# Performance work log

Measured on AMD Instinct MI355X. Metric: run time of the kernel, lower is better.

## Reference

```python
import jax, jax.numpy as jnp
import numpy as np

# Config matching init_kwargs: 63 single-grapheme tokens + optional blank -> C = 64,
# trivial (identity) lexicon, ngram = 0 (no transition model), allow_repeats = True.
# Under this config the GTN composition (target chain o lexicon -> tokens graph ->
# alignments, intersected with linear emission graph, forward_score) is exactly the
# CTC forward algorithm over the extended label sequence z = [blank, y1, blank, ...,
# yL, blank], with the s-2 -> s skip allowed for ALL non-blank states (allow_repeats).

B, T, C, L = 128, 3000, 64, 128
NEG = -1e30  # effective -inf, safe in fp32


def setup_inputs() -> dict:
    key = jax.random.key(0)
    k1, k2 = jax.random.split(key)
    inputs = jax.random.normal(k1, (B, T, C), dtype=jnp.float32)  # raw logits
    # target token ids in [0, C-2]; blank = C-1 is never a target
    targets = jax.random.randint(k2, (B, L), 0, C - 1, dtype=jnp.int32)
    return {"inputs": inputs, "targets": targets}


def reference(inputs, targets):
    Bv, Tv, Cv = inputs.shape
    Lv = targets.shape[1]
    S = 2 * Lv + 1
    blank = Cv - 1
    # transitions is None -> module applies log_softmax to inputs
    logp = jax.nn.log_softmax(inputs, axis=2)  # [B, T, C]
    # extended label sequence: blanks at even positions, targets at odd positions
    z = jnp.full((Bv, S), blank, dtype=jnp.int32).at[:, 1::2].set(targets)  # [B, S]
    # per-frame emission scores for each extended state: [B, T, S] -> [T, B, S]
    em = jnp.take_along_axis(logp, jnp.broadcast_to(z[:, None, :], (Bv, Tv, S)), axis=2)
    em = jnp.transpose(em, (1, 0, 2))
    # skip transition (s-2 -> s) allowed for every non-blank (odd) state because
    # allow_repeats=True (no z[s] != z[s-2] restriction)
    skip_ok = (jnp.arange(S) % 2 == 1)  # [S]

    alpha0 = (jnp.full((Bv, S), NEG, dtype=jnp.float32)
              .at[:, 0].set(em[0, :, 0])
              .at[:, 1].set(em[0, :, 1]))

    def step(alpha, e_t):
        a1 = jnp.pad(alpha[:, :-1], ((0, 0), (1, 0)), constant_values=NEG)
        a2 = jnp.pad(alpha[:, :-2], ((0, 0), (2, 0)), constant_values=NEG)
        a2 = jnp.where(skip_ok[None, :], a2, NEG)
        new = e_t + jax.scipy.special.logsumexp(jnp.stack([alpha, a1, a2], axis=0), axis=0)
        return new, None

    alphaT, _ = jax.lax.scan(step, alpha0, em[1:])  # [B, S]
    # accepting states: last label (S-2) and trailing blank (S-1)
    ll = jax.scipy.special.logsumexp(alphaT[:, S - 2:S], axis=1)  # [B]
    # reduction='none' -> scales = 1; forward returns torch.mean over batch
    return jnp.mean(-ll)
```

## Files before the change

kernel.cpp:

```cpp
#include <hip/hip_runtime.h>
#include <stdint.h>

#define BB 128
#define TT 3000
#define CC 64
#define LL 128
#define NEGf (-1e30f)
#define LOG2E 1.4426950408889634f
#define LN2f 0.6931471805599453f
#define F 12
#define NCH 250
#define NPH (NCH + 1)
#define NULLM (-30000)
#define LSE_BLOCKS 512

typedef float f32x2 __attribute__((ext_vector_type(2)));
typedef float f32x4 __attribute__((ext_vector_type(4)));

__device__ __forceinline__ float fexp2(float x){ return __builtin_amdgcn_exp2f(x); }
__device__ __forceinline__ float flog2(float x){ return __builtin_amdgcn_logf(x); }
__device__ __forceinline__ int dpp_shr1_i(int x, int old){
    return __builtin_amdgcn_update_dpp(old, x, 0x138, 0xF, 0xF, false);
}
__device__ __forceinline__ float dpp_shr1_f(float x, float old){
    int r = __builtin_amdgcn_update_dpp(__float_as_int(old), __float_as_int(x),
                                        0x138, 0xF, 0xF, false);
    return __int_as_float(r);
}
#define DPPMAXT(x,c) fmaxf((x),__int_as_float(__builtin_amdgcn_update_dpp(0,__float_as_int(x),(c),0xF,0xF,true)))
#define DPPADDT(x,c) ((x)+__int_as_float(__builtin_amdgcn_update_dpp(0,__float_as_int(x),(c),0xF,0xF,true)))
#define RED64(OP,x) { x=OP(x,0x111); x=OP(x,0x112); x=OP(x,0x114); x=OP(x,0x118); x=OP(x,0x142); x=OP(x,0x143); }

__global__ __launch_bounds__(512) void fused_kernel(const float* __restrict__ in,
                                                    const int* __restrict__ tgt,
                                                    float* __restrict__ lse,
                                                    float* __restrict__ ll2){
    __shared__ __align__(16) float emR[3][F][258];
    __shared__ __align__(16) float bndR[3][F][2];
    __shared__ __align__(16) float nullBnd[24];
    __shared__ float laL[3008];
    __shared__ float lbL[3008];
    if (blockIdx.x < BB) {
        const int b = blockIdx.x;
        const int wave = threadIdx.x >> 6;
        const int lane = threadIdx.x & 63;
        const float* fb = in + (size_t)b * TT * CC;
        const uint32_t em_base  = (uint32_t)(uintptr_t)&emR[0][0][0];
        const uint32_t bnd_base = (uint32_t)(uintptr_t)&bndR[0][0][0];

        if (wave < 2) {
            const int W = wave;
            __builtin_amdgcn_s_setprio(1);
            if (W == 0) {
                if (lane < 12) { nullBnd[2*lane] = __int_as_float(NULLM); nullBnd[2*lane+1] = 0.5f; }
                if (lane == 0) { bndR[0][0][0] = __int_as_float(NULLM); bndR[0][0][1] = 0.5f; }
                if (lane < 8) { laL[3000+lane] = NEGf; lbL[3000+lane] = 0.f; }
            }
            int a0m = NULLM, a1m = NULLM; float a0r = 0.5f, a1r = 0.5f;
            if (W == 0 && lane == 0) { a0m = 1; a0r = 0.5f; }
            const uint32_t em1_ad = em_base + (uint32_t)((64*W + lane) * 8);
            const uint32_t emB_ad = em_base + 1024u;
            const uint32_t nb_ad  = (uint32_t)(uintptr_t)&nullBnd[0];
            __syncthreads();
            for (int ph = 0; ph < NPH; ++ph) {
                const int x = ph - W;
                if (x >= 0 && x < NCH) {
                    const uint32_t buf = (uint32_t)(x % 3);
                    const uint32_t ra = em1_ad + buf*12384u;
                    const uint32_t rb = emB_ad + buf*12384u;
                    const uint32_t rq = W ? (bnd_base + buf*96u) : nb_ad;
                    f32x4 B4[6]; f32x2 E1[F], EB[F];
                    asm volatile("ds_read_b128 %0, %1 offset:0"  : "=v"(B4[0]) : "v"(rq));
                    asm volatile("ds_read_b128 %0, %1 offset:16" : "=v"(B4[1]) : "v"(rq));
                    asm volatile("ds_read_b128 %0, %1 offset:32" : "=v"(B4[2]) : "v"(rq));
                    asm volatile("ds_read_b128 %0, %1 offset:48" : "=v"(B4[3]) : "v"(rq));
                    asm volatile("ds_read_b128 %0, %1 offset:64" : "=v"(B4[4]) : "v"(rq));
                    asm volatile("ds_read_b128 %0, %1 offset:80" : "=v"(B4[5]) : "v"(rq));
                    asm volatile("ds_read_b64 %0, %1 offset:0"    : "=v"(E1[0]) : "v"(ra));
                    asm volatile("ds_read_b64 %0, %1 offset:0"    : "=v"(EB[0]) : "v"(rb));
                    asm volatile("ds_read_b64 %0, %1 offset:1032" : "=v"(E1[1]) : "v"(ra));
                    asm volatile("ds_read_b64 %0, %1 offset:1032" : "=v"(EB[1]) : "v"(rb));
                    asm volatile("ds_read_b64 %0, %1 offset:2064" : "=v"(E1[2]) : "v"(ra));
                    asm volatile("ds_read_b64 %0, %1 offset:2064" : "=v"(EB[2]) : "v"(rb));
                    int hm[F]; float hr[F];
                    #pragma unroll
                    for (int j = 0; j < F; ++j) {
                        if (j + 3 < F) {
                            asm volatile("ds_read_b64 %0, %1 offset:%2"
                                         : "=v"(E1[j+3]) : "v"(ra), "n"((j+3)*1032));
                            asm volatile("ds_read_b64 %0, %1 offset:%2"
                                         : "=v"(EB[j+3]) : "v"(rb), "n"((j+3)*1032));
                            asm volatile("s_waitcnt lgkmcnt(6)" ::: "memory");
                        } else if (j + 3 == F) {
                            asm volatile("s_waitcnt lgkmcnt(4)" ::: "memory");
                        } else if (j + 2 == F) {
                            asm volatile("s_waitcnt lgkmcnt(2)" ::: "memory");
                        } else {
                            asm volatile("s_waitcnt lgkmcnt(0)" ::: "memory");
                        }
                        __builtin_amdgcn_sched_barrier(0);
                        const int   bjm = __float_as_int((j&1) ? B4[j>>1].z : B4[j>>1].x);
                        const float bjr = (j&1) ? B4[j>>1].w : B4[j>>1].y;
                        const int   e1m = __float_as_int(E1[j].x); const float e1r = E1[j].y;
                        const int   ebm = __float_as_int(EB[j].x); const float ebr = EB[j].y;
                        int p1m = dpp_shr1_i(a1m, NULLM);
                        float p1r = dpp_shr1_f(a1r, 0.5f);
                        p1m = (lane == 0) ? bjm : p1m;
                        p1r = (lane == 0) ? bjr : p1r;
                        int Mt = (a0m > p1m) ? a0m : p1m;
                        float rs = ldexpf(a0r, a0m - Mt) + ldexpf(p1r, p1m - Mt);
                        int ui = __float_as_int(rs);
                        int n0m = Mt + ((ui >> 23) - 126) + ebm;
                        float n0r = __int_as_float((ui & 0x7FFFFF) | 0x3F000000) * ebr;
                        int Mu = (a1m > a0m) ? a1m : a0m; Mu = (Mu > p1m) ? Mu : p1m;
                        float ru = ldexpf(a1r, a1m - Mu) + ldexpf(a0r, a0m - Mu)
                                 + ldexpf(p1r, p1m - Mu);
                        int uj = __float_as_int(ru);
                        int n1m = Mu + ((uj >> 23) - 126) + e1m;
                        float n1r = __int_as_float((uj & 0x7FFFFF) | 0x3F000000) * e1r;
                        a0m = n0m; a0r = n0r; a1m = n1m; a1r = n1r;
                        hm[j] = a1m; hr[j] = a1r;
                    }
                    if (W == 0 && lane == 63) {
                        float* s0 = &bndR[x % 3][0][0];
                        #pragma unroll
                        for (int j = 0; j < F-1; ++j) {
                            s0[(j+1)*2] = __int_as_float(hm[j]); s0[(j+1)*2+1] = hr[j];
                        }
                        float* s1 = &bndR[(x+1) % 3][0][0];
                        s1[0] = __int_as_float(hm[F-1]); s1[1] = hr[F-1];
                    }
                    if (W == 1 && lane == 63) {
                        #pragma unroll
                        for (int j = 0; j < F; ++j)
                            laL[x*F + j] = (float)hm[j] + flog2(hr[j]);
                    }
                    asm volatile("s_waitcnt lgkmcnt(0)" ::: "memory");
                }
                __syncthreads();
            }
            __syncthreads();
            if (W == 0) {
                const int base = lane*47;
                float seg = 0.f;
                for (int k = 0; k < 47; ++k) seg += lbL[base+k];
                float inc = seg;
                #pragma unroll
                for (int d = 1; d < 64; d <<= 1) {
                    float t = __shfl_up(inc, d, 64);
                    if (lane >= d) inc += t;
                }
                float CBtot = __int_as_float(__builtin_amdgcn_readlane(__float_as_int(inc), 63));
                float ex = inc - seg;
                float cb = ex, gm = NEGf;
                for (int k = 0; k < 47; ++k) {
                    int idx = base+k;
                    cb += lbL[idx];
                    float g = laL[idx] + (CBtot - cb);
                    g = (idx == 2999) ? NEGf : g;
                    gm = fmaxf(gm, g);
                }
                RED64(DPPMAXT, gm);
                float gmax = __int_as_float(__builtin_amdgcn_readlane(__float_as_int(gm), 63));
                cb = ex; float se = 0.f;
                for (int k = 0; k < 47; ++k) {
                    int idx = base+k;
                    cb += lbL[idx];
                    float g = laL[idx] + (CBtot - cb);
                    g = (idx == 2999) ? NEGf : g;
                    se += fexp2(g - gmax);
                }
                RED64(DPPADDT, se);
                float S = __int_as_float(__builtin_amdgcn_readlane(__float_as_int(se), 63));
                float la256 = gmax + flog2(S);
                float la255f = laL[2999];
                float m = fmaxf(la255f, la256);
                float r = m + flog2(1.0f + fexp2(-fabsf(la255f - la256)));
                if (lane == 0) ll2[b] = r;
            }
        } else {
            const int p = wave - 2;
            const int t0 = tgt[b*LL + lane];
            const int t1 = tgt[b*LL + 64 + lane];
            float v0[2], v1[2], vb[2];
            auto loadc = [&](int cc){
                const float* cbase = fb + (size_t)cc * F * CC;
                #pragma unroll
                for (int k = 0; k < 2; ++k) {
                    const float* fr = cbase + (p + 6*k) * CC;
                    v0[k] = fr[t0]; v1[k] = fr[t1]; vb[k] = fr[63];
                }
            };
            auto storec = [&](int cc){
                const int buf = cc % 3;
                #pragma unroll
                for (int k = 0; k < 2; ++k) {
                    const int f = p + 6*k;
                    float x0 = v0[k] * LOG2E; float f0 = floorf(x0);
                    *(f32x2*)&emR[buf][f][2*lane] =
                        (f32x2){__int_as_float((int)f0 + 1), fexp2(x0 - f0 - 1.0f)};
                    float x1 = v1[k] * LOG2E; float f1 = floorf(x1);
                    *(f32x2*)&emR[buf][f][2*(64+lane)] =
                        (f32x2){__int_as_float((int)f1 + 1), fexp2(x1 - f1 - 1.0f)};
                    if (lane == 0) {
                        float xb = vb[k] * LOG2E; float fbl = floorf(xb);
                        *(f32x2*)&emR[buf][f][256] =
                            (f32x2){__int_as_float((int)fbl + 1), fexp2(xb - fbl - 1.0f)};
                        lbL[cc*F + f] = xb;
                    }
                }
            };
            loadc(0); storec(0); loadc(1);
            __syncthreads();
            for (int ph = 0; ph < NPH; ++ph) {
                if (ph + 1 < NCH) storec(ph + 1);
                if (ph + 2 < NCH) loadc(ph + 2);
                __syncthreads();
            }
            __syncthreads();
        }
        return;
    }
    int wv = (blockIdx.x - BB) * 8 + (threadIdx.x >> 6);
    int lane = threadIdx.x & 63;
    const int stride = LSE_BLOCKS * 8;
    for (int row = wv; row < BB * TT; row += stride) {
        float x = in[(size_t)row * CC + lane];
        float m = x;
        #pragma unroll
        for (int d = 32; d >= 1; d >>= 1) m = fmaxf(m, __shfl_xor(m, d, 64));
        float s = fexp2((x - m) * LOG2E);
        #pragma unroll
        for (int d = 32; d >= 1; d >>= 1) s += __shfl_xor(s, d, 64);
        if (lane == 0) lse[row] = m + flog2(s) * LN2f;
    }
}

__global__ __launch_bounds__(256) void bsum_kernel(const float* __restrict__ lse,
                                                   const float* __restrict__ ll2,
                                                   float* __restrict__ lossb) {
    __shared__ float red[256];
    int b = blockIdx.x;
    float s = 0.f;
    for (int i = threadIdx.x; i < TT; i += 256) s += lse[(size_t)b * TT + i];
    red[threadIdx.x] = s;
    __syncthreads();
    #pragma unroll
    for (int w = 128; w >= 1; w >>= 1) {
        if (threadIdx.x < w) red[threadIdx.x] += red[threadIdx.x + w];
        __syncthreads();
    }
    if (threadIdx.x == 0) lossb[b] = red[0] - ll2[b] * LN2f;
}

__global__ __launch_bounds__(64) void final_kernel(const float* __restrict__ lossb,
                                                   float* __restrict__ out) {
    int lane = threadIdx.x;
    float v = lossb[lane] + lossb[lane + 64];
    #pragma unroll
    for (int d = 32; d >= 1; d >>= 1) v += __shfl_xor(v, d, 64);
    if (lane == 0) out[0] = v / (float)BB;
}

extern "C" void kernel_launch(void* const* d_in, const int* in_sizes, int n_in,
                              void* d_out, int out_size, void* d_ws, size_t ws_size,
                              hipStream_t stream) {
    const float* in = (const float*)d_in[0];
    const int* tg = (const int*)d_in[1];
    float* out = (float*)d_out;
    float* lse = (float*)d_ws;
    float* ll2 = lse + (size_t)BB * TT;
    float* lossb = ll2 + BB;

    hipLaunchKernelGGL(fused_kernel, dim3(BB + LSE_BLOCKS), dim3(512), 0, stream,
                       in, tg, lse, ll2);
    hipLaunchKernelGGL(bsum_kernel, dim3(BB), dim3(256), 0, stream, lse, ll2, lossb);
    hipLaunchKernelGGL(final_kernel, dim3(1), dim3(64), 0, stream, lossb, out);
}
```

Before: 280.7 us.

## Replace per-chunk block barriers with LDS flag-based producer/consumer pipeline

Removes the __syncthreads per chunk between the two alpha-recursion waves and the six emission-loading waves. Coordination now uses LDS counters and flags with spin-wait polling, a 4-slot emission ring and a 5-slot boundary ring, so the two recursion waves can run a chunk apart without a full-block barrier. Emissions are stored as plain fp32 exp2 scales (one float per state instead of an exponent/mantissa pair), and each step folds the emission in with a multiply before renormalising. The log conversion of the saved alphas moves into the final reduction. The cost is extra polling traffic and s_sleep latency, plus a risk of subtle ordering bugs in the lock-free handoff.

After: 297.2 us. 5.9% more time.

```diff
diff --git a/kernel.cpp b/kernel.cpp
--- a/kernel.cpp
+++ b/kernel.cpp
@@ -10,7 +10,6 @@
 #define LN2f 0.6931471805599453f
 #define F 12
 #define NCH 250
-#define NPH (NCH + 1)
 #define NULLM (-30000)
 #define LSE_BLOCKS 512
 
@@ -30,16 +29,17 @@
 #define DPPMAXT(x,c) fmaxf((x),__int_as_float(__builtin_amdgcn_update_dpp(0,__float_as_int(x),(c),0xF,0xF,true)))
 #define DPPADDT(x,c) ((x)+__int_as_float(__builtin_amdgcn_update_dpp(0,__float_as_int(x),(c),0xF,0xF,true)))
 #define RED64(OP,x) { x=OP(x,0x111); x=OP(x,0x112); x=OP(x,0x114); x=OP(x,0x118); x=OP(x,0x142); x=OP(x,0x143); }
+#define MWALL() asm volatile("" ::: "memory")
 
 __global__ __launch_bounds__(512) void fused_kernel(const float* __restrict__ in,
                                                     const int* __restrict__ tgt,
                                                     float* __restrict__ lse,
                                                     float* __restrict__ ll2){
-    __shared__ __align__(16) float emR[3][F][258];
-    __shared__ __align__(16) float bndR[3][F][2];
-    __shared__ __align__(16) float nullBnd[24];
-    __shared__ float laL[3008];
+    __shared__ __align__(16) float emR[4][F][132];
+    __shared__ __align__(16) float bndR[5][F][2];
+    __shared__ __align__(16) f32x2 laP[3008];
     __shared__ float lbL[3008];
+    __shared__ int flg[8];
     if (blockIdx.x < BB) {
         const int b = blockIdx.x;
         const int wave = threadIdx.x >> 6;
@@ -47,177 +47,190 @@
         const float* fb = in + (size_t)b * TT * CC;
         const uint32_t em_base  = (uint32_t)(uintptr_t)&emR[0][0][0];
         const uint32_t bnd_base = (uint32_t)(uintptr_t)&bndR[0][0][0];
+        volatile int* cntp = (volatile int*)&flg[0];
+        volatile int* pap  = (volatile int*)&flg[4];
+        volatile int* pc1p = (volatile int*)&flg[5];
+        if (threadIdx.x == 0) {
+            #pragma unroll
+            for (int k = 0; k < 8; ++k) flg[k] = 0;
+        }
+        if (threadIdx.x < 8) {
+            laP[3000 + threadIdx.x] = (f32x2){__int_as_float(NULLM), 0.5f};
+            lbL[3000 + threadIdx.x] = 0.f;
+        }
+        __syncthreads();
 
         if (wave < 2) {
             const int W = wave;
             __builtin_amdgcn_s_setprio(1);
-            if (W == 0) {
-                if (lane < 12) { nullBnd[2*lane] = __int_as_float(NULLM); nullBnd[2*lane+1] = 0.5f; }
-                if (lane == 0) { bndR[0][0][0] = __int_as_float(NULLM); bndR[0][0][1] = 0.5f; }
-                if (lane < 8) { laL[3000+lane] = NEGf; lbL[3000+lane] = 0.f; }
-            }
             int a0m = NULLM, a1m = NULLM; float a0r = 0.5f, a1r = 0.5f;
-            if (W == 0 && lane == 0) { a0m = 1; a0r = 0.5f; }
-            const uint32_t em1_ad = em_base + (uint32_t)((64*W + lane) * 8);
-            const uint32_t emB_ad = em_base + 1024u;
-            const uint32_t nb_ad  = (uint32_t)(uintptr_t)&nullBnd[0];
-            __syncthreads();
-            for (int ph = 0; ph < NPH; ++ph) {
-                const int x = ph - W;
-                if (x >= 0 && x < NCH) {
-                    const uint32_t buf = (uint32_t)(x % 3);
-                    const uint32_t ra = em1_ad + buf*12384u;
-                    const uint32_t rb = emB_ad + buf*12384u;
-                    const uint32_t rq = W ? (bnd_base + buf*96u) : nb_ad;
-                    f32x4 B4[6]; f32x2 E1[F], EB[F];
+            if (W == 0 && lane == 0) a0m = 1;
+            int plm = NULLM; float plr = 0.5f;
+            for (int x = 0; x < NCH; ++x) {
+                const int slot4 = x & 3;
+                const int slot5 = x % 5;
+                if (W == 0) {
+                    const int need = 6 * ((x >> 2) + 1);
+                    int v = cntp[slot4];
+                    while (v < need) { __builtin_amdgcn_s_sleep(1); v = cntp[slot4]; }
+                } else {
+                    int v = *pap;
+                    while (v < x + 1) { __builtin_amdgcn_s_sleep(1); v = *pap; }
+                }
+                const uint32_t ra = em_base + (uint32_t)slot4*6336u + (64u*W + (uint32_t)lane)*4u;
+                const uint32_t rb = em_base + (uint32_t)slot4*6336u + 512u;
+                f32x4 B4[6];
+                if (W == 1) {
+                    const uint32_t rq = bnd_base + (uint32_t)slot5*96u;
                     asm volatile("ds_read_b128 %0, %1 offset:0"  : "=v"(B4[0]) : "v"(rq));
                     asm volatile("ds_read_b128 %0, %1 offset:16" : "=v"(B4[1]) : "v"(rq));
                     asm volatile("ds_read_b128 %0, %1 offset:32" : "=v"(B4[2]) : "v"(rq));
                     asm volatile("ds_read_b128 %0, %1 offset:48" : "=v"(B4[3]) : "v"(rq));
                     asm volatile("ds_read_b128 %0, %1 offset:64" : "=v"(B4[4]) : "v"(rq));
                     asm volatile("ds_read_b128 %0, %1 offset:80" : "=v"(B4[5]) : "v"(rq));
-                    asm volatile("ds_read_b64 %0, %1 offset:0"    : "=v"(E1[0]) : "v"(ra));
-                    asm volatile("ds_read_b64 %0, %1 offset:0"    : "=v"(EB[0]) : "v"(rb));
-                    asm volatile("ds_read_b64 %0, %1 offset:1032" : "=v"(E1[1]) : "v"(ra));
-                    asm volatile("ds_read_b64 %0, %1 offset:1032" : "=v"(EB[1]) : "v"(rb));
-                    asm volatile("ds_read_b64 %0, %1 offset:2064" : "=v"(E1[2]) : "v"(ra));
-                    asm volatile("ds_read_b64 %0, %1 offset:2064" : "=v"(EB[2]) : "v"(rb));
-                    int hm[F]; float hr[F];
+                } else {
                     #pragma unroll
-                    for (int j = 0; j < F; ++j) {
-                        if (j + 3 < F) {
-                            asm volatile("ds_read_b64 %0, %1 offset:%2"
-                                         : "=v"(E1[j+3]) : "v"(ra), "n"((j+3)*1032));
-                            asm volatile("ds_read_b64 %0, %1 offset:%2"
-                                         : "=v"(EB[j+3]) : "v"(rb), "n"((j+3)*1032));
-                            asm volatile("s_waitcnt lgkmcnt(6)" ::: "memory");
-                        } else if (j + 3 == F) {
-                            asm volatile("s_waitcnt lgkmcnt(4)" ::: "memory");
-                        } else if (j + 2 == F) {
-                            asm volatile("s_waitcnt lgkmcnt(2)" ::: "memory");
-                        } else {
-                            asm volatile("s_waitcnt lgkmcnt(0)" ::: "memory");
-                        }
-                        __builtin_amdgcn_sched_barrier(0);
-                        const int   bjm = __float_as_int((j&1) ? B4[j>>1].z : B4[j>>1].x);
-                        const float bjr = (j&1) ? B4[j>>1].w : B4[j>>1].y;
-                        const int   e1m = __float_as_int(E1[j].x); const float e1r = E1[j].y;
-                        const int   ebm = __float_as_int(EB[j].x); const float ebr = EB[j].y;
-                        int p1m = dpp_shr1_i(a1m, NULLM);
-                        float p1r = dpp_shr1_f(a1r, 0.5f);
-                        p1m = (lane == 0) ? bjm : p1m;
-                        p1r = (lane == 0) ? bjr : p1r;
-                        int Mt = (a0m > p1m) ? a0m : p1m;
-                        float rs = ldexpf(a0r, a0m - Mt) + ldexpf(p1r, p1m - Mt);
-                        int ui = __float_as_int(rs);
-                        int n0m = Mt + ((ui >> 23) - 126) + ebm;
-                        float n0r = __int_as_float((ui & 0x7FFFFF) | 0x3F000000) * ebr;
-                        int Mu = (a1m > a0m) ? a1m : a0m; Mu = (Mu > p1m) ? Mu : p1m;
-                        float ru = ldexpf(a1r, a1m - Mu) + ldexpf(a0r, a0m - Mu)
-                                 + ldexpf(p1r, p1m - Mu);
-                        int uj = __float_as_int(ru);
-                        int n1m = Mu + ((uj >> 23) - 126) + e1m;
-                        float n1r = __int_as_float((uj & 0x7FFFFF) | 0x3F000000) * e1r;
-                        a0m = n0m; a0r = n0r; a1m = n1m; a1r = n1r;
-                        hm[j] = a1m; hr[j] = a1r;
+                    for (int k = 0; k < 6; ++k)
+                        B4[k] = (f32x4){__int_as_float(NULLM), 0.5f, __int_as_float(NULLM), 0.5f};
+                }
+                float E[F], Bv[F]; int hm[F]; float hr[F];
+                asm volatile("ds_read_b32 %0, %1 offset:0"    : "=v"(E[0])  : "v"(ra));
+                asm volatile("ds_read_b32 %0, %1 offset:0"    : "=v"(Bv[0]) : "v"(rb));
+                asm volatile("ds_read_b32 %0, %1 offset:528"  : "=v"(E[1])  : "v"(ra));
+                asm volatile("ds_read_b32 %0, %1 offset:528"  : "=v"(Bv[1]) : "v"(rb));
+                asm volatile("ds_read_b32 %0, %1 offset:1056" : "=v"(E[2])  : "v"(ra));
+                asm volatile("ds_read_b32 %0, %1 offset:1056" : "=v"(Bv[2]) : "v"(rb));
+                #pragma unroll
+                for (int j = 0; j < F; ++j) {
+                    if (j + 3 < F) {
+                        asm volatile("ds_read_b32 %0, %1 offset:%2" : "=v"(E[j+3])  : "v"(ra), "n"((j+3)*528));
+                        asm volatile("ds_read_b32 %0, %1 offset:%2" : "=v"(Bv[j+3]) : "v"(rb), "n"((j+3)*528));
+                        asm volatile("s_waitcnt lgkmcnt(6)" ::: "memory");
+                    } else if (j + 3 == F) {
+                        asm volatile("s_waitcnt lgkmcnt(4)" ::: "memory");
+                    } else if (j + 2 == F) {
+                        asm volatile("s_waitcnt lgkmcnt(2)" ::: "memory");
+                    } else {
+                        asm volatile("s_waitcnt lgkmcnt(0)" ::: "memory");
                     }
-                    if (W == 0 && lane == 63) {
-                        float* s0 = &bndR[x % 3][0][0];
+                    __builtin_amdgcn_sched_barrier(0);
+                    const int   bjm = __float_as_int((j&1) ? B4[j>>1].z : B4[j>>1].x);
+                    const float bjr = (j&1) ? B4[j>>1].w : B4[j>>1].y;
+                    int   p1m = dpp_shr1_i(a1m, NULLM);
+                    float p1r = dpp_shr1_f(a1r, 0.5f);
+                    p1m = (lane == 0) ? bjm : p1m;
+                    p1r = (lane == 0) ? bjr : p1r;
+                    int Mt = (a0m > p1m) ? a0m : p1m;
+                    float rs = ldexpf(a0r, a0m - Mt) + ldexpf(p1r, p1m - Mt);
+                    float pr = rs * Bv[j];
+                    int ui = __float_as_int(pr);
+                    int n0m = Mt + ((ui >> 23) - 126);
+                    float n0r = __int_as_float((ui & 0x7FFFFF) | 0x3F000000);
+                    int Mu = (Mt > a1m) ? Mt : a1m;
+                    float ru = ldexpf(a1r, a1m - Mu) + ldexpf(a0r, a0m - Mu)
+                             + ldexpf(p1r, p1m - Mu);
+                    float qu = ru * E[j];
+                    int uj = __float_as_int(qu);
+                    int n1m = Mu + ((uj >> 23) - 126);
+                    float n1r = __int_as_float((uj & 0x7FFFFF) | 0x3F000000);
+                    a0m = n0m; a0r = n0r; a1m = n1m; a1r = n1r;
+                    hm[j] = a1m; hr[j] = a1r;
+                }
+                if (W == 0) {
+                    if (lane == 63) {
+                        float* s = &bndR[slot5][0][0];
+                        s[0] = __int_as_float(plm); s[1] = plr;
                         #pragma unroll
                         for (int j = 0; j < F-1; ++j) {
-                            s0[(j+1)*2] = __int_as_float(hm[j]); s0[(j+1)*2+1] = hr[j];
+                            s[(j+1)*2] = __int_as_float(hm[j]); s[(j+1)*2+1] = hr[j];
                         }
-                        float* s1 = &bndR[(x+1) % 3][0][0];
-                        s1[0] = __int_as_float(hm[F-1]); s1[1] = hr[F-1];
                     }
-                    if (W == 1 && lane == 63) {
+                    plm = hm[F-1]; plr = hr[F-1];
+                    MWALL();
+                    *pap = x + 1;
+                } else {
+                    if (lane == 63) {
                         #pragma unroll
                         for (int j = 0; j < F; ++j)
-                            laL[x*F + j] = (float)hm[j] + flog2(hr[j]);
+                            laP[x*F + j] = (f32x2){__int_as_float(hm[j]), hr[j]};
                     }
-                    asm volatile("s_waitcnt lgkmcnt(0)" ::: "memory");
-                }
-                __syncthreads();
-            }
-            __syncthreads();
-            if (W == 0) {
-                const int base = lane*47;
-                float seg = 0.f;
-                for (int k = 0; k < 47; ++k) seg += lbL[base+k];
-                float inc = seg;
-                #pragma unroll
-                for (int d = 1; d < 64; d <<= 1) {
-                    float t = __shfl_up(inc, d, 64);
-                    if (lane >= d) inc += t;
-                }
-                float CBtot = __int_as_float(__builtin_amdgcn_readlane(__float_as_int(inc), 63));
-                float ex = inc - seg;
-                float cb = ex, gm = NEGf;
-                for (int k = 0; k < 47; ++k) {
-                    int idx = base+k;
-                    cb += lbL[idx];
-                    float g = laL[idx] + (CBtot - cb);
-                    g = (idx == 2999) ? NEGf : g;
-                    gm = fmaxf(gm, g);
-                }
-                RED64(DPPMAXT, gm);
-                float gmax = __int_as_float(__builtin_amdgcn_readlane(__float_as_int(gm), 63));
-                cb = ex; float se = 0.f;
-                for (int k = 0; k < 47; ++k) {
-                    int idx = base+k;
-                    cb += lbL[idx];
-                    float g = laL[idx] + (CBtot - cb);
-                    g = (idx == 2999) ? NEGf : g;
-                    se += fexp2(g - gmax);
-                }
-                RED64(DPPADDT, se);
-                float S = __int_as_float(__builtin_amdgcn_readlane(__float_as_int(se), 63));
-                float la256 = gmax + flog2(S);
-                float la255f = laL[2999];
-                float m = fmaxf(la255f, la256);
-                float r = m + flog2(1.0f + fexp2(-fabsf(la255f - la256)));
-                if (lane == 0) ll2[b] = r;
+                    MWALL();
+                    *pc1p = x + 1;
+                }
             }
         } else {
             const int p = wave - 2;
             const int t0 = tgt[b*LL + lane];
             const int t1 = tgt[b*LL + 64 + lane];
-            float v0[2], v1[2], vb[2];
-            auto loadc = [&](int cc){
-                const float* cbase = fb + (size_t)cc * F * CC;
-                #pragma unroll
-                for (int k = 0; k < 2; ++k) {
-                    const float* fr = cbase + (p + 6*k) * CC;
-                    v0[k] = fr[t0]; v1[k] = fr[t1]; vb[k] = fr[63];
-                }
-            };
-            auto storec = [&](int cc){
-                const int buf = cc % 3;
-                #pragma unroll
-                for (int k = 0; k < 2; ++k) {
-                    const int f = p + 6*k;
-                    float x0 = v0[k] * LOG2E; float f0 = floorf(x0);
-                    *(f32x2*)&emR[buf][f][2*lane] =
-                        (f32x2){__int_as_float((int)f0 + 1), fexp2(x0 - f0 - 1.0f)};
-                    float x1 = v1[k] * LOG2E; float f1 = floorf(x1);
-                    *(f32x2*)&emR[buf][f][2*(64+lane)] =
-                        (f32x2){__int_as_float((int)f1 + 1), fexp2(x1 - f1 - 1.0f)};
-                    if (lane == 0) {
-                        float xb = vb[k] * LOG2E; float fbl = floorf(xb);
-                        *(f32x2*)&emR[buf][f][256] =
-                            (f32x2){__int_as_float((int)fbl + 1), fexp2(xb - fbl - 1.0f)};
-                        lbL[cc*F + f] = xb;
-                    }
-                }
-            };
-            loadc(0); storec(0); loadc(1);
-            __syncthreads();
-            for (int ph = 0; ph < NPH; ++ph) {
-                if (ph + 1 < NCH) storec(ph + 1);
-                if (ph + 2 < NCH) loadc(ph + 2);
-                __syncthreads();
-            }
-            __syncthreads();
+            float Av0[2], Av1[2], Avb[2], Bw0[2], Bw1[2], Bwb[2];
+#define LOADP(S, c) { const float* cb_ = fb + (size_t)(c)*(F*CC); \
+            _Pragma("unroll") for (int k = 0; k < 2; ++k) { \
+                const float* fr_ = cb_ + (p + 6*k)*CC; \
+                S##0[k] = fr_[t0]; S##1[k] = fr_[t1]; S##b[k] = fr_[63]; } }
+#define STORP(S, c) { const int buf_ = (c) & 3; \
+            _Pragma("unroll") for (int k = 0; k < 2; ++k) { \
+                const int f_ = p + 6*k; \
+                emR[buf_][f_][lane]    = fexp2(S##0[k]*LOG2E); \
+                emR[buf_][f_][64+lane] = fexp2(S##1[k]*LOG2E); \
+                if (lane == 0) { float xb_ = S##b[k]*LOG2E; \
+                    emR[buf_][f_][128] = fexp2(xb_); lbL[(c)*F + f_] = xb_; } } }
+#define PPOLL(c) { const int need_ = (c) - 3; int v_ = *pc1p; \
+            while (v_ < need_) { __builtin_amdgcn_s_sleep(2); v_ = *pc1p; } }
+            LOADP(Av, 0);
+            for (int c = 0; c < NCH; c += 2) {
+                if (c + 1 < NCH) LOADP(Bw, c + 1);
+                MWALL();
+                PPOLL(c); STORP(Av, c); MWALL();
+                atomicAdd((int*)&flg[c & 3], 1);
+                if (c + 1 < NCH) {
+                    if (c + 2 < NCH) LOADP(Av, c + 2);
+                    MWALL();
+                    PPOLL(c + 1); STORP(Bw, c + 1); MWALL();
+                    atomicAdd((int*)&flg[(c + 1) & 3], 1);
+                }
+            }
+        }
+        __syncthreads();
+        if (wave == 0) {
+            const int base = lane * 47;
+            float seg = 0.f;
+            for (int k = 0; k < 47; ++k) seg += lbL[base + k];
+            float inc = seg;
+            #pragma unroll
+            for (int d = 1; d < 64; d <<= 1) {
+                float t = __shfl_up(inc, d, 64);
+                if (lane >= d) inc += t;
+            }
+            float CBtot = __int_as_float(__builtin_amdgcn_readlane(__float_as_int(inc), 63));
+            float ex = inc - seg;
+            float cb = ex, gm = NEGf;
+            for (int k = 0; k < 47; ++k) {
+                int idx = base + k;
+                cb += lbL[idx];
+                f32x2 lp = laP[idx];
+                float g = (float)__float_as_int(lp.x) + flog2(lp.y) + (CBtot - cb);
+                g = (idx == 2999) ? NEGf : g;
+                gm = fmaxf(gm, g);
+            }
+            RED64(DPPMAXT, gm);
+            float gmax = __int_as_float(__builtin_amdgcn_readlane(__float_as_int(gm), 63));
+            cb = ex; float se = 0.f;
+            for (int k = 0; k < 47; ++k) {
+                int idx = base + k;
+                cb += lbL[idx];
+                f32x2 lp = laP[idx];
+                float g = (float)__float_as_int(lp.x) + flog2(lp.y) + (CBtot - cb);
+                g = (idx == 2999) ? NEGf : g;
+                se += fexp2(g - gmax);
+            }
+            RED64(DPPADDT, se);
+            float S = __int_as_float(__builtin_amdgcn_readlane(__float_as_int(se), 63));
+            float la256 = gmax + flog2(S);
+            f32x2 lp9 = laP[2999];
+            float la255f = (float)__float_as_int(lp9.x) + flog2(lp9.y);
+            float m = fmaxf(la255f, la256);
+            float r = m + flog2(1.0f + fexp2(-fabsf(la255f - la256)));
+            if (lane == 0) ll2[b] = r;
         }
         return;
     }
```
